# Optimization experiments

Measured on AMD Instinct MI355X. Metric: run time of the kernel, lower is better.

The kernel has to match this reference:

```python
import jax, jax.numpy as jnp
import numpy as np

B, N = 32, 200000          # images, flattened candidates per image (anchors*classes)
NUM_CLASSES = 21           # VOC-style class count for the label-offset trick
CONF_THR = 0.05            # cfg.PRED_CONF_THR
NMS_THR = 0.5              # cfg.PRED_NMS_THR
TOPK = 500                 # cfg.PRED_SELECT_TOPK
KEEP_MAX = 100             # cfg.PRED_NMS_KEEP


def setup_inputs() -> dict:
    key = jax.random.key(0)
    k1, k2, k3, k4 = jax.random.split(key, 4)
    pscores = jax.random.uniform(k1, (B, N), dtype=jnp.float32)
    # well-formed ltrb boxes in [0,1]: right>left, bottom>top
    xy1 = jax.random.uniform(k2, (B, N, 2), dtype=jnp.float32) * 0.8
    wh = jax.random.uniform(k3, (B, N, 2), dtype=jnp.float32) * 0.2 + 0.01
    pboxes = jnp.concatenate([xy1, xy1 + wh], axis=-1)
    plabels = jax.random.randint(k4, (B, N), 0, NUM_CLASSES)
    return {"pscores": pscores, "pboxes": pboxes, "plabels": plabels}


def _box_iou(a, b):
    # a: [K,4], b: [K,4] ltrb -> [K,K] pairwise IoU (torchvision convention)
    lt = jnp.maximum(a[:, None, :2], b[None, :, :2])
    rb = jnp.minimum(a[:, None, 2:], b[None, :, 2:])
    wh = jnp.clip(rb - lt, 0.0)
    inter = wh[..., 0] * wh[..., 1]
    area_a = (a[:, 2] - a[:, 0]) * (a[:, 3] - a[:, 1])
    area_b = (b[:, 2] - b[:, 0]) * (b[:, 3] - b[:, 1])
    return inter / (area_a[:, None] + area_b[None, :] - inter)


def _greedy_nms(iou_mat, valid, thr):
    # candidates are pre-sorted by score descending (lax.top_k output order)
    K = valid.shape[0]
    idxs = jnp.arange(K)

    def body(keep, i):
        suppressed = jnp.any(keep & (iou_mat[i] > thr) & (idxs < i))
        k = valid[i] & (~suppressed)
        return keep.at[i].set(k), None

    keep, _ = jax.lax.scan(body, jnp.zeros((K,), dtype=bool), idxs)
    return keep


def reference(pscores, pboxes, plabels):
    # ---- threshold + top-k pre-selection (mask_pos AND mask_topk) ----
    scores_k, idx = jax.lax.top_k(pscores, TOPK)          # [B,K] sorted desc
    valid = scores_k > CONF_THR                           # equivalent to mask_pos & mask_topk
    bidx = jnp.arange(B)[:, None]
    boxes_k = pboxes[bidx, idx]                           # [B,K,4]
    labels_k = plabels[bidx, idx]                         # [B,K]

    # ---- multi-class NMS via label offset trick (batched_nms) ----
    max_coord = jnp.max(jnp.where(valid[..., None], boxes_k, 0.0), axis=(1, 2))  # [B]
    offsets = labels_k.astype(boxes_k.dtype) * (max_coord[:, None] + 1.0)
    boxes_nms = boxes_k + offsets[..., None]              # [B,K,4]

    iou = jax.vmap(_box_iou)(boxes_nms, boxes_nms)        # [B,K,K]
    keep = jax.vmap(lambda m, v: _greedy_nms(m, v, NMS_THR))(iou, valid)  # [B,K] bool

    # ---- keep[:num_max] per batch ----
    rank = jnp.cumsum(keep.astype(jnp.int32), axis=1)
    keep = keep & (rank <= KEEP_MAX)

    # compact kept entries to front (jnp.argsort is stable -> score order preserved), pad to KEEP_MAX
    order = jnp.argsort(jnp.where(keep, 0, 1), axis=1)[:, :KEEP_MAX]       # [B,KEEP]
    out_valid = jnp.take_along_axis(keep, order, axis=1)                    # [B,KEEP]
    boxes2 = jnp.take_along_axis(boxes_k, order[..., None], axis=1) * out_valid[..., None]
    scores2 = jnp.take_along_axis(scores_k, order, axis=1) * out_valid
    labels2 = jnp.where(out_valid, jnp.take_along_axis(labels_k, order, axis=1), -1)
    ids_batch2 = jnp.where(out_valid, jnp.arange(B)[:, None], -1)
    return ids_batch2, boxes2, labels2, scores2, out_valid
```

## Files before the change

### kernel.cpp

```cpp
#include <hip/hip_runtime.h>
#include <stdint.h>

#pragma clang fp contract(off)

#define BB 32
#define NN 200000
#define N4 50000
#define KK 500
#define KEEPN 100
#define CONF 0.05f
#define NMSTHR 0.5f
#define SLICES 8
#define SLICE_F4 6250
#define LBINS 8192
#define LSHIFT 19
#define LOCAL_CAP 2048
#define OUT_CAP 576
#define M_CAP (SLICES * OUT_CAP)
#define OK0 0xBF733333u

typedef unsigned long long u64;


__device__ __forceinline__ unsigned int ordkey(float s) {
    unsigned int u = __float_as_uint(s);
    return (u & 0x80000000u) ? ~u : (u | 0x80000000u);
}

__device__ __forceinline__ void wappend(bool pred, u64 key, u64* keys, int* lcnt, int lane) {
    u64 bm = __ballot(pred);
    int pre = __popcll(bm & ((1ULL << lane) - 1ULL));
    int tt  = __popcll(bm);
    int base = 0;
    if (lane == 0 && tt > 0) base = atomicAdd(lcnt, tt);
    base = __shfl(base, 0);
    if (pred) { int pos = base + pre; if (pos < LOCAL_CAP) keys[pos] = key; }
}

__global__ __launch_bounds__(1024) void select_kernel(const float4* __restrict__ ps4,
                                                      u64* __restrict__ cand,
                                                      unsigned int* __restrict__ cnts) {
    __shared__ unsigned int hist[LBINS];
    __shared__ u64 keys[LOCAL_CAP];
    __shared__ unsigned int h[256];
    __shared__ unsigned int wsum[16];
    __shared__ u64 wmin[16], wmax[16];
    __shared__ u64 s_prefix;
    __shared__ unsigned int s_t13, s_region, s_cntgt;
    __shared__ int s_lcnt, s_sc, s_shift0;

    const int b = blockIdx.y, x = blockIdx.x;
    const int tid = threadIdx.x, lane = tid & 63, wv = tid >> 6;
    const float4* p = ps4 + (size_t)b * N4 + (size_t)x * SLICE_F4;
    const int ebase = x * (SLICE_F4 * 4);

    if (tid == 0) s_lcnt = 0;
    __syncthreads();

    for (int i = tid; i < SLICE_F4; i += 1024) {
        float4 v = p[i];
        int n = ebase + (i << 2);
        unsigned int ux = ordkey(v.x), uy = ordkey(v.y);
        unsigned int uz = ordkey(v.z), uw = ordkey(v.w);
        wappend(ux >= OK0, ((u64)ux << 32) | (unsigned int)(~(unsigned int)(n)),     keys, &s_lcnt, lane);
        wappend(uy >= OK0, ((u64)uy << 32) | (unsigned int)(~(unsigned int)(n + 1)), keys, &s_lcnt, lane);
        wappend(uz >= OK0, ((u64)uz << 32) | (unsigned int)(~(unsigned int)(n + 2)), keys, &s_lcnt, lane);
        wappend(uw >= OK0, ((u64)uw << 32) | (unsigned int)(~(unsigned int)(n + 3)), keys, &s_lcnt, lane);
    }
    __syncthreads();
    int m = s_lcnt;

    if (m < KK || m > LOCAL_CAP) {
        for (int i = tid; i < LBINS; i += 1024) hist[i] = 0;
        __syncthreads();
        for (int i = tid; i < SLICE_F4; i += 1024) {
            float4 v = p[i];
            atomicAdd(&hist[ordkey(v.x) >> LSHIFT], 1u);
            atomicAdd(&hist[ordkey(v.y) >> LSHIFT], 1u);
            atomicAdd(&hist[ordkey(v.z) >> LSHIFT], 1u);
            atomicAdd(&hist[ordkey(v.w) >> LSHIFT], 1u);
        }
        __syncthreads();
        unsigned int v8[8], tot = 0;
        for (int j = 0; j < 8; ++j) { v8[j] = hist[tid * 8 + j]; tot += v8[j]; }
        unsigned int sfx = tot;
        for (int off = 1; off < 64; off <<= 1) {
            unsigned int t2 = __shfl_down(sfx, off);
            sfx += (lane + off < 64) ? t2 : 0u;
        }
        if (lane == 0) wsum[wv] = sfx;
        __syncthreads();
        unsigned int wafter = 0;
        for (int w2 = wv + 1; w2 < 16; ++w2) wafter += wsum[w2];
        unsigned int sn = wafter + (sfx - tot);
        for (int j = 7; j >= 0; --j) {
            unsigned int s = sn + v8[j];
            if (s >= (unsigned)KK && sn < (unsigned)KK) s_t13 = (unsigned)(tid * 8 + j);
            sn = s;
        }
        if (tid == 0) s_lcnt = 0;
        __syncthreads();
        const unsigned int t13 = s_t13;
        for (int i = tid; i < SLICE_F4; i += 1024) {
            float4 v = p[i];
            int n = ebase + (i << 2);
            unsigned int u;
            u = ordkey(v.x); if ((u >> LSHIFT) >= t13) { int pos = atomicAdd(&s_lcnt, 1);
                if (pos < LOCAL_CAP) keys[pos] = ((u64)u << 32) | (unsigned int)(~(unsigned int)(n)); }
            u = ordkey(v.y); if ((u >> LSHIFT) >= t13) { int pos = atomicAdd(&s_lcnt, 1);
                if (pos < LOCAL_CAP) keys[pos] = ((u64)u << 32) | (unsigned int)(~(unsigned int)(n + 1)); }
            u = ordkey(v.z); if ((u >> LSHIFT) >= t13) { int pos = atomicAdd(&s_lcnt, 1);
                if (pos < LOCAL_CAP) keys[pos] = ((u64)u << 32) | (unsigned int)(~(unsigned int)(n + 2)); }
            u = ordkey(v.w); if ((u >> LSHIFT) >= t13) { int pos = atomicAdd(&s_lcnt, 1);
                if (pos < LOCAL_CAP) keys[pos] = ((u64)u << 32) | (unsigned int)(~(unsigned int)(n + 3)); }
        }
        __syncthreads();
        m = s_lcnt; if (m > LOCAL_CAP) m = LOCAL_CAP;
    }

    u64 thr; int seln;
    if (m <= OUT_CAP) {
        thr = 0ULL; seln = m;
    } else {
        u64 kmn = ~0ULL, kmx = 0ULL;
        for (int i = tid; i < m; i += 1024) {
            u64 k = keys[i];
            kmn = k < kmn ? k : kmn; kmx = k > kmx ? k : kmx;
        }
        for (int off = 32; off > 0; off >>= 1) {
            u64 a = __shfl_down(kmn, off), c = __shfl_down(kmx, off);
            if (lane + off < 64) { kmn = a < kmn ? a : kmn; kmx = c > kmx ? c : kmx; }
        }
        if (lane == 0) { wmin[wv] = kmn; wmax[wv] = kmx; }
        __syncthreads();
        if (tid == 0) {
            u64 mn = wmin[0], mx = wmax[0];
            for (int w2 = 1; w2 < 16; ++w2) {
                mn = wmin[w2] < mn ? wmin[w2] : mn;
                mx = wmax[w2] > mx ? wmax[w2] : mx;
            }
            u64 diff = mn ^ mx;
            int hb = 63 - __builtin_clzll(diff | 1ULL);
            int st = (hb >> 3) << 3;
            s_shift0 = st;
            s_prefix = (st == 56) ? 0ULL : (mx >> (st + 8));
            s_cntgt = 0u;
        }
        __syncthreads();
        int shift = s_shift0;
        for (; shift >= 0; shift -= 8) {
            if (tid < 256) h[tid] = 0u;
            __syncthreads();
            u64 pref = s_prefix;
            unsigned int cg = s_cntgt;
            for (int i = tid; i < m; i += 1024) {
                u64 k = keys[i];
                bool match = (shift == 56) || ((k >> (shift + 8)) == pref);
                if (match) atomicAdd(&h[(unsigned int)((k >> shift) & 0xFF)], 1u);
            }
            __syncthreads();
            if (wv == 0) {
                unsigned int b4[4]; unsigned int lt = 0;
                for (int j = 0; j < 4; ++j) { b4[j] = h[lane * 4 + j]; lt += b4[j]; }
                unsigned int sx = lt;
                for (int off = 1; off < 64; off <<= 1) {
                    unsigned int t2 = __shfl_down(sx, off);
                    sx += (lane + off < 64) ? t2 : 0u;
                }
                unsigned int after = sx - lt;
                unsigned int target = (unsigned)KK - cg;
                unsigned int sn2 = after;
                for (int j = 3; j >= 0; --j) {
                    unsigned int s = sn2 + b4[j];
                    if (s >= target && sn2 < target) {
                        unsigned int bin = (unsigned)(lane * 4 + j);
                        s_region = b4[j];
                        s_cntgt = cg + sn2;
                        s_prefix = (shift == 56) ? (u64)bin : ((pref << 8) | (u64)bin);
                    }
                    sn2 = s;
                }
            }
            __syncthreads();
            if (s_cntgt + s_region <= (unsigned)OUT_CAP) break;
        }
        if (shift < 0) shift = 0;
        thr = s_prefix << shift;
        seln = (int)(s_cntgt + s_region);
    }
    (void)seln;

    if (tid == 0) s_sc = 0;
    __syncthreads();
    u64* outslice = cand + (size_t)(b * SLICES + x) * OUT_CAP;
    for (int r0 = 0; r0 < LOCAL_CAP / 1024; ++r0) {
        int i = tid + r0 * 1024;
        u64 k = (i < m) ? keys[i] : 0ULL;
        bool pq = (i < m) && (k >= thr);
        u64 mb = __ballot(pq);
        int pre = __popcll(mb & ((1ULL << lane) - 1ULL));
        int tt = __popcll(mb);
        int base = 0;
        if (lane == 0 && tt > 0) base = atomicAdd(&s_sc, tt);
        base = __shfl(base, 0);
        if (pq && base + pre < OUT_CAP) outslice[base + pre] = k;
    }
    __syncthreads();
    if (tid == 0) {
        int c = s_sc; if (c > OUT_CAP) c = OUT_CAP;
        cnts[b * SLICES + x] = (unsigned)c;
    }
}

__global__ __launch_bounds__(1024) void final_kernel(const float* __restrict__ pboxes,
                                                     const int* __restrict__ plabels,
                                                     const u64* __restrict__ cand,
                                                     const unsigned int* __restrict__ cnts,
                                                     float* __restrict__ out) {
    __shared__ u64 kbuf[M_CAP];
    __shared__ u64 sel[OUT_CAP];
    __shared__ float sboxes[KK * 5];
    __shared__ float sscore[KK];
    __shared__ int slabel[KK];
    __shared__ int clist[KK];
    __shared__ unsigned int h[256];
    __shared__ int ccnt[21], coff[22], cfill[21];
    __shared__ int scnt[SLICES];
    __shared__ u64 validw[8];
    __shared__ u64 sremv[8];
    __shared__ u64 s_km;
    __shared__ int kept[KEEPN];
    __shared__ float wred[16];
    __shared__ u64 wmin[16], wmax[16];
    __shared__ int soff[SLICES + 1];
    __shared__ u64 s_prefix;
    __shared__ unsigned int s_region, s_cntgt;
    __shared__ int s_sc, s_nk, s_stop, s_shift0;
    __shared__ float s_maxc;

    const int b = blockIdx.x;
    const int tid = threadIdx.x;
    const int lane = tid & 63;
    const int wv = tid >> 6;

    if (tid < SLICES) {
        int c = (int)cnts[b * SLICES + tid];
        if (c > OUT_CAP) c = OUT_CAP;
        scnt[tid] = c;
    }
    __syncthreads();
    if (tid == 0) {
        int acc = 0;
        for (int s = 0; s < SLICES; ++s) { soff[s] = acc; acc += scnt[s]; }
        soff[SLICES] = acc;
    }
    __syncthreads();
    int m = soff[SLICES];
    for (int s = 0; s < SLICES; ++s) {
        int off = soff[s], len = soff[s + 1] - off;
        const u64* src = cand + (size_t)(b * SLICES + s) * OUT_CAP;
        for (int i = tid; i < len; i += 1024) kbuf[off + i] = src[i];
    }
    __syncthreads();

    u64 thr; int seln;
    if (m <= OUT_CAP) {
        thr = 0ULL; seln = m;
    } else {
        u64 kmn = ~0ULL, kmx = 0ULL;
        for (int i = tid; i < m; i += 1024) {
            u64 k = kbuf[i];
            kmn = k < kmn ? k : kmn; kmx = k > kmx ? k : kmx;
        }
        for (int off = 32; off > 0; off >>= 1) {
            u64 a = __shfl_down(kmn, off), c = __shfl_down(kmx, off);
            if (lane + off < 64) { kmn = a < kmn ? a : kmn; kmx = c > kmx ? c : kmx; }
        }
        if (lane == 0) { wmin[wv] = kmn; wmax[wv] = kmx; }
        __syncthreads();
        if (tid == 0) {
            u64 mn = wmin[0], mx = wmax[0];
            for (int w2 = 1; w2 < 16; ++w2) {
                mn = wmin[w2] < mn ? wmin[w2] : mn;
                mx = wmax[w2] > mx ? wmax[w2] : mx;
            }
            u64 diff = mn ^ mx;
            int hb = 63 - __builtin_clzll(diff | 1ULL);
            int st = (hb >> 3) << 3;
            s_shift0 = st;
            s_prefix = (st == 56) ? 0ULL : (mx >> (st + 8));
            s_cntgt = 0u;
        }
        __syncthreads();
        int shift = s_shift0;
        for (; shift >= 0; shift -= 8) {
            if (tid < 256) h[tid] = 0u;
            __syncthreads();
            u64 pref = s_prefix;
            unsigned int cg = s_cntgt;
            for (int i = tid; i < m; i += 1024) {
                u64 k = kbuf[i];
                bool match = (shift == 56) || ((k >> (shift + 8)) == pref);
                if (match) atomicAdd(&h[(unsigned int)((k >> shift) & 0xFF)], 1u);
            }
            __syncthreads();
            if (wv == 0) {
                unsigned int b4[4]; unsigned int lt = 0;
                for (int j = 0; j < 4; ++j) { b4[j] = h[lane * 4 + j]; lt += b4[j]; }
                unsigned int sx = lt;
                for (int off = 1; off < 64; off <<= 1) {
                    unsigned int t2 = __shfl_down(sx, off);
                    sx += (lane + off < 64) ? t2 : 0u;
                }
                unsigned int after = sx - lt;
                unsigned int target = (unsigned)KK - cg;
                unsigned int sn2 = after;
                for (int j = 3; j >= 0; --j) {
                    unsigned int s = sn2 + b4[j];
                    if (s >= target && sn2 < target) {
                        unsigned int bin = (unsigned)(lane * 4 + j);
                        s_region = b4[j];
                        s_cntgt = cg + sn2;
                        s_prefix = (shift == 56) ? (u64)bin : ((pref << 8) | (u64)bin);
                    }
                    sn2 = s;
                }
            }
            __syncthreads();
            if (s_cntgt + s_region <= (unsigned)OUT_CAP) break;
        }
        if (shift < 0) shift = 0;
        thr = s_prefix << shift;
        seln = (int)(s_cntgt + s_region);
    }

    if (tid == 0) s_sc = 0;
    __syncthreads();
    for (int r0 = 0; r0 < (M_CAP + 1023) / 1024; ++r0) {
        int i = tid + r0 * 1024;
        u64 k = (i < m) ? kbuf[i] : 0ULL;
        bool pq = (i < m) && (k >= thr);
        u64 mb = __ballot(pq);
        int pre = __popcll(mb & ((1ULL << lane) - 1ULL));
        int tt = __popcll(mb);
        int base = 0;
        if (lane == 0 && tt > 0) base = atomicAdd(&s_sc, tt);
        base = __shfl(base, 0);
        if (pq) sel[base + pre] = k;
    }
    __syncthreads();

    u64 myk = (tid < seln) ? sel[tid] : 0ULL;
    float mysc = -1.0f; int mylab = 0;
    float4 mybx = make_float4(0.0f, 0.0f, 0.0f, 0.0f);
    if (tid < seln) {
        unsigned int lo = (unsigned int)myk;
        unsigned int hi = (unsigned int)(myk >> 32);
        int idx = (int)(~lo);
        unsigned int bits = (hi & 0x80000000u) ? (hi & 0x7FFFFFFFu) : ~hi;
        mysc = __uint_as_float(bits);
        mybx = *(const float4*)(pboxes + (((size_t)b * NN + (size_t)idx) << 2));
        mylab = plabels[(size_t)b * NN + idx];
    }
    if (tid < KK) {
        sscore[tid] = -1.0f; slabel[tid] = 0;
        sboxes[tid * 5 + 0] = 0.0f; sboxes[tid * 5 + 1] = 0.0f;
        sboxes[tid * 5 + 2] = 0.0f; sboxes[tid * 5 + 3] = 0.0f;
    }

    int r = 0;
    if ((tid & ~63) < seln) {
        for (int base = 0; base < seln; base += 64) {
            int i2 = base + lane;
            u64 other = (i2 < seln) ? sel[i2] : 0ULL;
            unsigned int olo = (unsigned int)other, ohi = (unsigned int)(other >> 32);
            int lim = seln - base; if (lim > 64) lim = 64;
            for (int t2 = 0; t2 < lim; ++t2) {
                unsigned int blo = (unsigned int)__builtin_amdgcn_readlane((int)olo, t2);
                unsigned int bhi = (unsigned int)__builtin_amdgcn_readlane((int)ohi, t2);
                u64 o = ((u64)bhi << 32) | (u64)blo;
                r += (o > myk) ? 1 : 0;
            }
        }
    }
    __syncthreads();
    if (tid < seln && r < KK) {
        sboxes[r * 5 + 0] = mybx.x; sboxes[r * 5 + 1] = mybx.y;
        sboxes[r * 5 + 2] = mybx.z; sboxes[r * 5 + 3] = mybx.w;
        sscore[r] = mysc; slabel[r] = mylab;
    }
    __syncthreads();

    float sc = (tid < KK) ? sscore[tid] : -1.0f;
    bool vq = (tid < KK) && (sc > CONF);
    u64 bm = __ballot(vq);
    if (lane == 0 && wv < 8) validw[wv] = bm;
    float lm = vq ? fmaxf(fmaxf(sboxes[tid * 5 + 0], sboxes[tid * 5 + 1]),
                          fmaxf(sboxes[tid * 5 + 2], sboxes[tid * 5 + 3])) : 0.0f;
    for (int off = 32; off > 0; off >>= 1) lm = fmaxf(lm, __shfl_down(lm, off));
    if (lane == 0) wred[wv] = lm;
    __syncthreads();
    if (tid < 64) {
        float x = (tid < 16) ? wred[tid] : 0.0f;
        for (int off = 8; off > 0; off >>= 1) x = fmaxf(x, __shfl_down(x, off));
        if (tid == 0) s_maxc = x;
    }
    if (tid < 21) { ccnt[tid] = 0; cfill[tid] = 0; }
    if (tid < 8) sremv[tid] = 0ULL;
    if (tid == 0) { s_nk = 0; s_stop = 0; }
    __syncthreads();
    if (tid < KK) atomicAdd(&ccnt[slabel[tid]], 1);
    __syncthreads();
    if (tid == 0) {
        int acc = 0;
        for (int c = 0; c < 21; ++c) { coff[c] = acc; acc += ccnt[c]; }
        coff[21] = acc;
    }
    __syncthreads();
    if (tid < KK) {
        int c = slabel[tid];
        int pos = atomicAdd(&cfill[c], 1);
        clist[coff[c] + pos] = tid;
    }
    u64 (*msk)[512] = (u64(*)[512])kbuf;
    for (int i = tid; i < 8 * 512; i += 1024) ((u64*)kbuf)[i] = 0ULL;
    __syncthreads();

    float ap1 = s_maxc + 1.0f;
    if (tid < KK) {
        int c = slabel[tid];
        int n = ccnt[c], base0 = coff[c];
        float aoff = (float)c * ap1;
        float a0 = sboxes[tid * 5 + 0] + aoff, a1 = sboxes[tid * 5 + 1] + aoff;
        float a2 = sboxes[tid * 5 + 2] + aoff, a3 = sboxes[tid * 5 + 3] + aoff;
        float areaA = (a2 - a0) * (a3 - a1);
        for (int q = 0; q < n; ++q) {
            int j = clist[base0 + q];
            float b0 = sboxes[j * 5 + 0] + aoff, b1f = sboxes[j * 5 + 1] + aoff;
            float b2f = sboxes[j * 5 + 2] + aoff, b3f = sboxes[j * 5 + 3] + aoff;
            float lt0 = fmaxf(a0, b0), lt1 = fmaxf(a1, b1f);
            float rb0 = fminf(a2, b2f), rb1 = fminf(a3, b3f);
            float ww = fmaxf(rb0 - lt0, 0.0f), hh = fmaxf(rb1 - lt1, 0.0f);
            float inter = ww * hh;
            float areaB = (b2f - b0) * (b3f - b1f);
            float iou = inter / (areaA + areaB - inter);
            if (iou > NMSTHR) msk[j >> 6][tid] |= (1ULL << (j & 63));
        }
    }
    __syncthreads();

    for (int c = 0; c < 8; ++c) {
        if (wv == 0) {
            u64 rowc = msk[c][c * 64 + lane];
            unsigned int rl = (unsigned int)rowc, rh = (unsigned int)(rowc >> 32);
            u64 cur = sremv[c];
            u64 vv = validw[c];
            u64 km = 0ULL;
            int nk = s_nk;
            for (int j = 0; j < 64; ++j) {
                if (nk >= KEEPN) break;
                bool alive = (((vv >> j) & 1ULL) != 0ULL) && (((cur >> j) & 1ULL) == 0ULL);
                if (alive) {
                    if (lane == 0) kept[nk] = c * 64 + j;
                    u64 rv = ((u64)(unsigned int)__builtin_amdgcn_readlane((int)rh, j) << 32)
                           |  (u64)(unsigned int)__builtin_amdgcn_readlane((int)rl, j);
                    cur |= rv;
                    km |= (1ULL << j);
                    ++nk;
                }
            }
            if (lane == 0) { s_km = km; s_nk = nk; sremv[c] = cur; s_stop = (nk >= KEEPN) ? 1 : 0; }
        }
        __syncthreads();
        if (s_stop || c == 7) break;
        if (wv > c && wv < 8) {
            u64 km = s_km;
            u64 v = ((km >> lane) & 1ULL) ? msk[wv][c * 64 + lane] : 0ULL;
            for (int off2 = 32; off2 > 0; off2 >>= 1) v |= __shfl_xor(v, off2);
            if (lane == 0) sremv[wv] |= v;
        }
        __syncthreads();
    }

    if (tid < KEEPN) {
        const int O_BOX = BB * KEEPN;
        const int O_LAB = BB * KEEPN * 5;
        const int O_SCO = BB * KEEPN * 6;
        const int O_VAL = BB * KEEPN * 7;
        bool q = tid < s_nk;
        int i = q ? kept[tid] : 0;
        int g = b * KEEPN + tid;
        out[g]                 = q ? (float)b : -1.0f;
        out[O_BOX + g * 4 + 0] = q ? sboxes[i * 5 + 0] : 0.0f;
        out[O_BOX + g * 4 + 1] = q ? sboxes[i * 5 + 1] : 0.0f;
        out[O_BOX + g * 4 + 2] = q ? sboxes[i * 5 + 2] : 0.0f;
        out[O_BOX + g * 4 + 3] = q ? sboxes[i * 5 + 3] : 0.0f;
        out[O_LAB + g]         = q ? (float)slabel[i] : -1.0f;
        out[O_SCO + g]         = q ? sscore[i] : 0.0f;
        out[O_VAL + g]         = q ? 1.0f : 0.0f;
    }
}

extern "C" void kernel_launch(void* const* d_in, const int* in_sizes, int n_in,
                              void* d_out, int out_size, void* d_ws, size_t ws_size,
                              hipStream_t stream) {
    const float* pscores = (const float*)d_in[0];
    const float* pboxes  = (const float*)d_in[1];
    const int*   plabels = (const int*)d_in[2];
    float* out = (float*)d_out;

    uint8_t* ws = (uint8_t*)d_ws;
    u64*          cand = (u64*)(ws + 0);
    unsigned int* cnts = (unsigned int*)(ws + 1179648);

    select_kernel<<<dim3(SLICES, BB), 1024, 0, stream>>>((const float4*)pscores, cand, cnts);
    final_kernel<<<BB, 1024, 0, stream>>>(pboxes, plabels, cand, cnts, out);
}
```

Measured before the change: 218.6 us.

## Replace iterative radix select with single 4096-bin histogram bucket sort in final kernel

The final per-image kernel no longer copies all slice candidates into shared memory and runs a multi-pass 8-bit radix select followed by an all-pairs rank. It builds a single 4096-bin histogram over a 12-bit window of the keys, finds the bin containing the 500th element from prefix sums, scatters the qualifying keys into bucketed positions, and ranks each key only against the other keys in its own bin. The old radix-select path is kept as a fallback for skewed histograms (a bin holding more than 64 keys) or overflow, and it now rereads candidates from global memory instead of a shared copy. This trades several barrier-heavy passes and O(n^2) ranking for one histogram pass plus small per-bin scans, at the cost of rereading candidates from global memory and a larger shared histogram.

```diff
diff --git a/kernel.cpp b/kernel.cpp
--- a/kernel.cpp
+++ b/kernel.cpp
@@ -16,7 +16,7 @@
 #define LSHIFT 19
 #define LOCAL_CAP 2048
 #define OUT_CAP 576
-#define M_CAP (SLICES * OUT_CAP)
+#define TMPCAP 640
 #define OK0 0xBF733333u
 
 typedef unsigned long long u64;
@@ -217,102 +217,191 @@
                                                      const u64* __restrict__ cand,
                                                      const unsigned int* __restrict__ cnts,
                                                      float* __restrict__ out) {
-    __shared__ u64 kbuf[M_CAP];
-    __shared__ u64 sel[OUT_CAP];
+    __shared__ u64 pool[4736];
     __shared__ float sboxes[KK * 5];
     __shared__ float sscore[KK];
     __shared__ int slabel[KK];
     __shared__ int clist[KK];
-    __shared__ unsigned int h[256];
+    __shared__ int scnt[SLICES];
+    __shared__ u64 wmin[16], wmax[16];
+    __shared__ unsigned int wsum[16], wmaxh[16];
+    __shared__ float wred[16];
     __shared__ int ccnt[21], coff[22], cfill[21];
-    __shared__ int scnt[SLICES];
-    __shared__ u64 validw[8];
-    __shared__ u64 sremv[8];
-    __shared__ u64 s_km;
+    __shared__ u64 validw[8], sremv[8], s_km;
     __shared__ int kept[KEEPN];
-    __shared__ float wred[16];
-    __shared__ u64 wmin[16], wmax[16];
-    __shared__ int soff[SLICES + 1];
-    __shared__ u64 s_prefix;
+    __shared__ u64 s_kmn, s_kmx, s_prefix;
     __shared__ unsigned int s_region, s_cntgt;
-    __shared__ int s_sc, s_nk, s_stop, s_shift0;
+    __shared__ int s_shift, s_thrbin, s_selupper, s_fb, s_bsh, s_sc, s_nk, s_stop;
     __shared__ float s_maxc;
+
+    unsigned int* hist = (unsigned int*)pool;
+    unsigned int* pfx  = ((unsigned int*)pool) + 4096;
+    u64* tmp = (u64*)((char*)pool + 32768);
 
     const int b = blockIdx.x;
     const int tid = threadIdx.x;
     const int lane = tid & 63;
     const int wv = tid >> 6;
+    const u64* cb = cand + (size_t)b * SLICES * OUT_CAP;
 
     if (tid < SLICES) {
         int c = (int)cnts[b * SLICES + tid];
-        if (c > OUT_CAP) c = OUT_CAP;
-        scnt[tid] = c;
-    }
+        scnt[tid] = c > OUT_CAP ? OUT_CAP : c;
+    }
+    if (tid == 0) { s_thrbin = 0; s_fb = 0; s_nk = 0; s_stop = 0; }
+    __syncthreads();
+
+    for (int i = tid; i < 4096; i += 1024) hist[i] = 0u;
+    u64 kmn = ~0ULL, kmx = 0ULL;
+    for (int s = 0; s < SLICES; ++s) {
+        if (tid < scnt[s]) {
+            u64 k = cb[(size_t)s * OUT_CAP + tid];
+            kmn = k < kmn ? k : kmn; kmx = k > kmx ? k : kmx;
+        }
+    }
+    for (int off = 32; off > 0; off >>= 1) {
+        u64 a = __shfl_down(kmn, off), c2 = __shfl_down(kmx, off);
+        if (lane + off < 64) { kmn = a < kmn ? a : kmn; kmx = c2 > kmx ? c2 : kmx; }
+    }
+    if (lane == 0) { wmin[wv] = kmn; wmax[wv] = kmx; }
     __syncthreads();
     if (tid == 0) {
-        int acc = 0;
-        for (int s = 0; s < SLICES; ++s) { soff[s] = acc; acc += scnt[s]; }
-        soff[SLICES] = acc;
-    }
-    __syncthreads();
-    int m = soff[SLICES];
+        u64 mn = wmin[0], mx = wmax[0];
+        for (int w2 = 1; w2 < 16; ++w2) {
+            mn = wmin[w2] < mn ? wmin[w2] : mn;
+            mx = wmax[w2] > mx ? wmax[w2] : mx;
+        }
+        s_kmn = mn; s_kmx = mx;
+        u64 diff = mn ^ mx;
+        int hb = 63 - __builtin_clzll(diff | 1ULL);
+        int sh = hb - 11; if (sh < 0) sh = 0;
+        s_shift = sh;
+    }
+    __syncthreads();
+    const int shift = s_shift;
+
     for (int s = 0; s < SLICES; ++s) {
-        int off = soff[s], len = soff[s + 1] - off;
-        const u64* src = cand + (size_t)(b * SLICES + s) * OUT_CAP;
-        for (int i = tid; i < len; i += 1024) kbuf[off + i] = src[i];
-    }
-    __syncthreads();
-
-    u64 thr; int seln;
-    if (m <= OUT_CAP) {
-        thr = 0ULL; seln = m;
+        if (tid < scnt[s]) {
+            u64 k = cb[(size_t)s * OUT_CAP + tid];
+            atomicAdd(&hist[(unsigned int)((k >> shift) & 0xFFFu)], 1u);
+        }
+    }
+    __syncthreads();
+
+    unsigned int h4[4]; unsigned int lt = 0, hm = 0;
+    const int g0 = tid << 2;
+    for (int j = 0; j < 4; ++j) { h4[j] = hist[g0 + j]; lt += h4[j]; hm = h4[j] > hm ? h4[j] : hm; }
+    unsigned int sfx = lt;
+    for (int off = 1; off < 64; off <<= 1) {
+        unsigned int t2 = __shfl_down(sfx, off);
+        sfx += (lane + off < 64) ? t2 : 0u;
+    }
+    unsigned int mh = hm;
+    for (int off = 1; off < 64; off <<= 1) {
+        unsigned int t2 = __shfl_down(mh, off);
+        if (lane + off < 64) mh = t2 > mh ? t2 : mh;
+    }
+    if (lane == 0) { wsum[wv] = sfx; wmaxh[wv] = mh; }
+    __syncthreads();
+    unsigned int wafter = 0;
+    for (int w2 = wv + 1; w2 < 16; ++w2) wafter += wsum[w2];
+    unsigned int run = wafter + (sfx - lt);
+    for (int j = 3; j >= 0; --j) {
+        pfx[g0 + j] = run;
+        if (run < (unsigned)KK && run + h4[j] >= (unsigned)KK) s_thrbin = g0 + j;
+        run += h4[j];
+    }
+    if (tid == 0) {
+        unsigned int mmh = 0;
+        for (int w2 = 0; w2 < 16; ++w2) mmh = wmaxh[w2] > mmh ? wmaxh[w2] : mmh;
+        if (mmh > 64u) s_fb = 1;
+    }
+    __syncthreads();
+    if (tid == 0) {
+        int tb = s_thrbin;
+        unsigned int su = pfx[tb] + hist[tb];
+        s_selupper = (int)su;
+        if (su > (unsigned)TMPCAP) s_fb = 1;
+    }
+    if (tid < KK) {
+        sscore[tid] = -1.0f; slabel[tid] = 0;
+        sboxes[tid * 5 + 0] = 0.0f; sboxes[tid * 5 + 1] = 0.0f;
+        sboxes[tid * 5 + 2] = 0.0f; sboxes[tid * 5 + 3] = 0.0f;
+    }
+    __syncthreads();
+
+    if (!s_fb) {
+        const int thrbin = s_thrbin;
+        for (int s = 0; s < SLICES; ++s) {
+            if (tid < scnt[s]) {
+                u64 k = cb[(size_t)s * OUT_CAP + tid];
+                unsigned int g = (unsigned int)((k >> shift) & 0xFFFu);
+                if ((int)g >= thrbin) {
+                    unsigned int p = atomicAdd(&pfx[g], 1u);
+                    if (p < (unsigned)TMPCAP) tmp[p] = k;
+                }
+            }
+        }
+        __syncthreads();
+        int nr = s_selupper; if (nr > TMPCAP) nr = TMPCAP;
+        if (tid < nr) {
+            u64 k = tmp[tid];
+            unsigned int g = (unsigned int)((k >> shift) & 0xFFFu);
+            unsigned int c = hist[g];
+            unsigned int base = pfx[g] - c;
+            unsigned int lo = (unsigned int)k, hi = (unsigned int)(k >> 32);
+            int idx = (int)(~lo);
+            unsigned int bits = (hi & 0x80000000u) ? (hi & 0x7FFFFFFFu) : ~hi;
+            float msc = __uint_as_float(bits);
+            const float4 bx = *(const float4*)(pboxes + (((size_t)b * NN + (size_t)idx) << 2));
+            int lab = plabels[(size_t)b * NN + idx];
+            int rank = 0;
+            for (unsigned int q = 0; q < c; ++q) {
+                u64 o = tmp[base + q];
+                rank += (o > k) ? 1 : 0;
+            }
+            int fin = (int)base + rank;
+            if (fin < KK) {
+                sboxes[fin * 5 + 0] = bx.x; sboxes[fin * 5 + 1] = bx.y;
+                sboxes[fin * 5 + 2] = bx.z; sboxes[fin * 5 + 3] = bx.w;
+                sscore[fin] = msc; slabel[fin] = lab;
+            }
+        }
+        __syncthreads();
     } else {
-        u64 kmn = ~0ULL, kmx = 0ULL;
-        for (int i = tid; i < m; i += 1024) {
-            u64 k = kbuf[i];
-            kmn = k < kmn ? k : kmn; kmx = k > kmx ? k : kmx;
-        }
-        for (int off = 32; off > 0; off >>= 1) {
-            u64 a = __shfl_down(kmn, off), c = __shfl_down(kmx, off);
-            if (lane + off < 64) { kmn = a < kmn ? a : kmn; kmx = c > kmx ? c : kmx; }
-        }
-        if (lane == 0) { wmin[wv] = kmn; wmax[wv] = kmx; }
-        __syncthreads();
         if (tid == 0) {
-            u64 mn = wmin[0], mx = wmax[0];
-            for (int w2 = 1; w2 < 16; ++w2) {
-                mn = wmin[w2] < mn ? wmin[w2] : mn;
-                mx = wmax[w2] > mx ? wmax[w2] : mx;
-            }
+            u64 mn = s_kmn, mx = s_kmx;
             u64 diff = mn ^ mx;
             int hb = 63 - __builtin_clzll(diff | 1ULL);
             int st = (hb >> 3) << 3;
-            s_shift0 = st;
+            s_bsh = st;
             s_prefix = (st == 56) ? 0ULL : (mx >> (st + 8));
             s_cntgt = 0u;
         }
         __syncthreads();
-        int shift = s_shift0;
-        for (; shift >= 0; shift -= 8) {
-            if (tid < 256) h[tid] = 0u;
+        int sh2 = s_bsh;
+        for (; sh2 >= 0; sh2 -= 8) {
+            if (tid < 256) hist[tid] = 0u;
             __syncthreads();
             u64 pref = s_prefix;
             unsigned int cg = s_cntgt;
-            for (int i = tid; i < m; i += 1024) {
-                u64 k = kbuf[i];
-                bool match = (shift == 56) || ((k >> (shift + 8)) == pref);
-                if (match) atomicAdd(&h[(unsigned int)((k >> shift) & 0xFF)], 1u);
+            for (int s = 0; s < SLICES; ++s) {
+                if (tid < scnt[s]) {
+                    u64 k = cb[(size_t)s * OUT_CAP + tid];
+                    bool match = (sh2 == 56) || ((k >> (sh2 + 8)) == pref);
+                    if (match) atomicAdd(&hist[(unsigned int)((k >> sh2) & 0xFF)], 1u);
+                }
             }
             __syncthreads();
             if (wv == 0) {
-                unsigned int b4[4]; unsigned int lt = 0;
-                for (int j = 0; j < 4; ++j) { b4[j] = h[lane * 4 + j]; lt += b4[j]; }
-                unsigned int sx = lt;
+                unsigned int b4[4]; unsigned int lt2 = 0;
+                for (int j = 0; j < 4; ++j) { b4[j] = hist[lane * 4 + j]; lt2 += b4[j]; }
+                unsigned int sx = lt2;
                 for (int off = 1; off < 64; off <<= 1) {
                     unsigned int t2 = __shfl_down(sx, off);
                     sx += (lane + off < 64) ? t2 : 0u;
                 }
-                unsigned int after = sx - lt;
+                unsigned int after = sx - lt2;
                 unsigned int target = (unsigned)KK - cg;
                 unsigned int sn2 = after;
                 for (int j = 3; j >= 0; --j) {
@@ -321,7 +410,7 @@
                         unsigned int bin = (unsigned)(lane * 4 + j);
                         s_region = b4[j];
                         s_cntgt = cg + sn2;
-                        s_prefix = (shift == 56) ? (u64)bin : ((pref << 8) | (u64)bin);
+                        s_prefix = (sh2 == 56) ? (u64)bin : ((pref << 8) | (u64)bin);
                     }
                     sn2 = s;
                 }
@@ -329,67 +418,54 @@
             __syncthreads();
             if (s_cntgt + s_region <= (unsigned)OUT_CAP) break;
         }
-        if (shift < 0) shift = 0;
-        thr = s_prefix << shift;
-        seln = (int)(s_cntgt + s_region);
-    }
-
-    if (tid == 0) s_sc = 0;
-    __syncthreads();
-    for (int r0 = 0; r0 < (M_CAP + 1023) / 1024; ++r0) {
-        int i = tid + r0 * 1024;
-        u64 k = (i < m) ? kbuf[i] : 0ULL;
-        bool pq = (i < m) && (k >= thr);
-        u64 mb = __ballot(pq);
-        int pre = __popcll(mb & ((1ULL << lane) - 1ULL));
-        int tt = __popcll(mb);
-        int base = 0;
-        if (lane == 0 && tt > 0) base = atomicAdd(&s_sc, tt);
-        base = __shfl(base, 0);
-        if (pq) sel[base + pre] = k;
-    }
-    __syncthreads();
-
-    u64 myk = (tid < seln) ? sel[tid] : 0ULL;
-    float mysc = -1.0f; int mylab = 0;
-    float4 mybx = make_float4(0.0f, 0.0f, 0.0f, 0.0f);
-    if (tid < seln) {
-        unsigned int lo = (unsigned int)myk;
-        unsigned int hi = (unsigned int)(myk >> 32);
-        int idx = (int)(~lo);
-        unsigned int bits = (hi & 0x80000000u) ? (hi & 0x7FFFFFFFu) : ~hi;
-        mysc = __uint_as_float(bits);
-        mybx = *(const float4*)(pboxes + (((size_t)b * NN + (size_t)idx) << 2));
-        mylab = plabels[(size_t)b * NN + idx];
-    }
-    if (tid < KK) {
-        sscore[tid] = -1.0f; slabel[tid] = 0;
-        sboxes[tid * 5 + 0] = 0.0f; sboxes[tid * 5 + 1] = 0.0f;
-        sboxes[tid * 5 + 2] = 0.0f; sboxes[tid * 5 + 3] = 0.0f;
-    }
-
-    int r = 0;
-    if ((tid & ~63) < seln) {
-        for (int base = 0; base < seln; base += 64) {
-            int i2 = base + lane;
-            u64 other = (i2 < seln) ? sel[i2] : 0ULL;
-            unsigned int olo = (unsigned int)other, ohi = (unsigned int)(other >> 32);
-            int lim = seln - base; if (lim > 64) lim = 64;
-            for (int t2 = 0; t2 < lim; ++t2) {
-                unsigned int blo = (unsigned int)__builtin_amdgcn_readlane((int)olo, t2);
-                unsigned int bhi = (unsigned int)__builtin_amdgcn_readlane((int)ohi, t2);
-                u64 o = ((u64)bhi << 32) | (u64)blo;
-                r += (o > myk) ? 1 : 0;
-            }
-        }
-    }
-    __syncthreads();
-    if (tid < seln && r < KK) {
-        sboxes[r * 5 + 0] = mybx.x; sboxes[r * 5 + 1] = mybx.y;
-        sboxes[r * 5 + 2] = mybx.z; sboxes[r * 5 + 3] = mybx.w;
-        sscore[r] = mysc; slabel[r] = mylab;
-    }
-    __syncthreads();
+        if (sh2 < 0) sh2 = 0;
+        u64 thr2 = s_prefix << sh2;
+        int seln = (int)(s_cntgt + s_region);
+        if (seln > TMPCAP) seln = TMPCAP;
+        if (tid == 0) s_sc = 0;
+        __syncthreads();
+        for (int s = 0; s < SLICES; ++s) {
+            u64 k = 0ULL; bool pq = false;
+            if (tid < scnt[s]) { k = cb[(size_t)s * OUT_CAP + tid]; pq = (k >= thr2); }
+            u64 mb = __ballot(pq);
+            int pre = __popcll(mb & ((1ULL << lane) - 1ULL));
+            int tt = __popcll(mb);
+            int bse = 0;
+            if (lane == 0 && tt > 0) bse = atomicAdd(&s_sc, tt);
+            bse = __shfl(bse, 0);
+            if (pq) { int pos = bse + pre; if (pos < TMPCAP) tmp[pos] = k; }
+        }
+        __syncthreads();
+        u64 myk = (tid < seln) ? tmp[tid] : 0ULL;
+        int r = 0;
+        if ((tid & ~63) < seln) {
+            for (int base = 0; base < seln; base += 64) {
+                int i2 = base + lane;
+                u64 other = (i2 < seln) ? tmp[i2] : 0ULL;
+                unsigned int olo = (unsigned int)other, ohi = (unsigned int)(other >> 32);
+                int lim = seln - base; if (lim > 64) lim = 64;
+                for (int t2 = 0; t2 < lim; ++t2) {
+                    unsigned int blo = (unsigned int)__builtin_amdgcn_readlane((int)olo, t2);
+                    unsigned int bhi = (unsigned int)__builtin_amdgcn_readlane((int)ohi, t2);
+                    u64 o = ((u64)bhi << 32) | (u64)blo;
+                    r += (o > myk) ? 1 : 0;
+                }
+            }
+        }
+        __syncthreads();
+        if (tid < seln && r < KK) {
+            unsigned int lo = (unsigned int)myk, hi = (unsigned int)(myk >> 32);
+            int idx = (int)(~lo);
+            unsigned int bits = (hi & 0x80000000u) ? (hi & 0x7FFFFFFFu) : ~hi;
+            float msc = __uint_as_float(bits);
+            const float4 bx = *(const float4*)(pboxes + (((size_t)b * NN + (size_t)idx) << 2));
+            int lab = plabels[(size_t)b * NN + idx];
+            sboxes[r * 5 + 0] = bx.x; sboxes[r * 5 + 1] = bx.y;
+            sboxes[r * 5 + 2] = bx.z; sboxes[r * 5 + 3] = bx.w;
+            sscore[r] = msc; slabel[r] = lab;
+        }
+        __syncthreads();
+    }
 
     float sc = (tid < KK) ? sscore[tid] : -1.0f;
     bool vq = (tid < KK) && (sc > CONF);
@@ -407,7 +483,6 @@
     }
     if (tid < 21) { ccnt[tid] = 0; cfill[tid] = 0; }
     if (tid < 8) sremv[tid] = 0ULL;
-    if (tid == 0) { s_nk = 0; s_stop = 0; }
     __syncthreads();
     if (tid < KK) atomicAdd(&ccnt[slabel[tid]], 1);
     __syncthreads();
@@ -422,8 +497,8 @@
         int pos = atomicAdd(&cfill[c], 1);
         clist[coff[c] + pos] = tid;
     }
-    u64 (*msk)[512] = (u64(*)[512])kbuf;
-    for (int i = tid; i < 8 * 512; i += 1024) ((u64*)kbuf)[i] = 0ULL;
+    u64 (*msk)[512] = (u64(*)[512])pool;
+    for (int i = tid; i < 8 * 512; i += 1024) ((u64*)pool)[i] = 0ULL;
     __syncthreads();
 
     float ap1 = s_maxc + 1.0f;
```

Result: faster. 201.5 us (-7.8%).
